# Performance work log

Measured on AMD Instinct MI355X. Metric: run time of the kernel, lower is better.

Reference implementation:

```python
import jax, jax.numpy as jnp
import numpy as np

B, D, H = 16384, 2048, 16
EPS = 1e-5


def setup_inputs() -> dict:
    key = jax.random.key(0)
    ks = jax.random.split(key, 14)
    s = 0.02
    return {
        "e_a": jax.random.normal(ks[0], (B, D), jnp.float32),
        "e_b": jax.random.normal(ks[1], (B, D), jnp.float32),
        "w_in_ab": jax.random.normal(ks[2], (3 * D, D), jnp.float32) * s,
        "b_in_ab": jnp.zeros((3 * D,), jnp.float32),
        "w_out_ab": jax.random.normal(ks[3], (D, D), jnp.float32) * s,
        "b_out_ab": jnp.zeros((D,), jnp.float32),
        "w_in_ba": jax.random.normal(ks[4], (3 * D, D), jnp.float32) * s,
        "b_in_ba": jnp.zeros((3 * D,), jnp.float32),
        "w_out_ba": jax.random.normal(ks[5], (D, D), jnp.float32) * s,
        "b_out_ba": jnp.zeros((D,), jnp.float32),
        "gamma_a": jnp.ones((D,), jnp.float32),
        "beta_a": jnp.zeros((D,), jnp.float32),
        "gamma_b": jnp.ones((D,), jnp.float32),
        "beta_b": jnp.zeros((D,), jnp.float32),
    }


def _mha_seq1(q_in, kv_in, w_in, b_in, w_out, b_out):
    """torch nn.MultiheadAttention with seq_len=1 for both query and key."""
    b, d = q_in.shape
    hd = d // H
    wq, wk, wv = jnp.split(w_in, 3, axis=0)
    bq, bk, bv = jnp.split(b_in, 3)
    q = (q_in @ wq.T + bq).reshape(b, H, hd)
    k = (kv_in @ wk.T + bk).reshape(b, H, hd)
    v = (kv_in @ wv.T + bv).reshape(b, H, hd)
    scores = jnp.sum(q * k, axis=-1) / jnp.sqrt(jnp.asarray(hd, q.dtype))  # (B,H)
    w = jax.nn.softmax(scores[..., None], axis=-1)  # (B,H,1) == ones (single key)
    attn = (w * v).reshape(b, d)
    out = attn @ w_out.T + b_out
    attn_w = jnp.mean(w, axis=1)[:, None, :]  # (B,1,1), averaged over heads
    return out, attn_w


def _layernorm(x, g, b):
    m = jnp.mean(x, axis=-1, keepdims=True)
    v = jnp.mean((x - m) ** 2, axis=-1, keepdims=True)
    return (x - m) / jnp.sqrt(v + EPS) * g + b


def reference(e_a, e_b, w_in_ab, b_in_ab, w_out_ab, b_out_ab,
              w_in_ba, b_in_ba, w_out_ba, b_out_ba,
              gamma_a, beta_a, gamma_b, beta_b):
    a_attn, attn_w_a = _mha_seq1(e_a, e_b, w_in_ab, b_in_ab, w_out_ab, b_out_ab)
    b_attn, _ = _mha_seq1(e_b, e_a, w_in_ba, b_in_ba, w_out_ba, b_out_ba)
    e_a_prime = _layernorm(e_a + a_attn, gamma_a, beta_a)
    e_b_prime = _layernorm(e_b + b_attn, gamma_b, beta_b)
    return (e_a_prime, e_b_prime, attn_w_a)
```

## Files before the change

### kernel.cpp

```cpp
#include <hip/hip_runtime.h>
#include <hip/hip_bf16.h>
#include <stdint.h>
#include <stddef.h>


static constexpr int B_ROWS = 16384;
static constexpr int DIM    = 2048;
static constexpr float EPS  = 1e-5f;

typedef __bf16 bf16_t;
typedef __bf16 bf16x8 __attribute__((ext_vector_type(8)));
typedef float  f32x4  __attribute__((ext_vector_type(4)));

__global__ __launch_bounds__(256) void k_f32_to_bf16(const float* __restrict__ in,
                                                     bf16_t* __restrict__ out) {
  size_t i = ((size_t)blockIdx.x * 256 + threadIdx.x) * 8;
  f32x4 a = *(const f32x4*)(in + i);
  f32x4 b = *(const f32x4*)(in + i + 4);
  bf16x8 o;
  o[0] = (bf16_t)a[0]; o[1] = (bf16_t)a[1]; o[2] = (bf16_t)a[2]; o[3] = (bf16_t)a[3];
  o[4] = (bf16_t)b[0]; o[5] = (bf16_t)b[1]; o[6] = (bf16_t)b[2]; o[7] = (bf16_t)b[3];
  *(bf16x8*)(out + i) = o;
}

__global__ __launch_bounds__(256) void k_transpose_bf16(const float* __restrict__ W,
                                                        bf16_t* __restrict__ Wt,
                                                        int n) {
  __shared__ float t[32][33];
  const int bx = blockIdx.x * 32, by = blockIdx.y * 32;
  const int tx = threadIdx.x & 31, ty = threadIdx.x >> 5;
  #pragma unroll
  for (int r = ty; r < 32; r += 8)
    t[r][tx] = W[(size_t)(by + r) * n + bx + tx];
  __syncthreads();
  #pragma unroll
  for (int r = ty; r < 32; r += 8)
    Wt[(size_t)(bx + r) * n + by + tx] = (bf16_t)t[tx][r];
}

__global__ __launch_bounds__(256) void k_bias_combine(const float* __restrict__ wout,
                                                      const float* __restrict__ bv,
                                                      const float* __restrict__ bout,
                                                      float* __restrict__ bc, int n) {
  const int i = blockIdx.x;
  const float* row = wout + (size_t)i * n;
  float s = 0.f;
  for (int k = threadIdx.x; k < n; k += 256) s += row[k] * bv[k];
  #pragma unroll
  for (int o = 32; o; o >>= 1) s += __shfl_down(s, o, 64);
  __shared__ float red[4];
  if ((threadIdx.x & 63) == 0) red[threadIdx.x >> 6] = s;
  __syncthreads();
  if (threadIdx.x == 0) bc[i] = red[0] + red[1] + red[2] + red[3] + bout[i];
}

__device__ inline void gld_lds16(const bf16_t* g, bf16_t* l) {
  __builtin_amdgcn_global_load_lds(
      (const __attribute__((address_space(1))) void*)g,
      (__attribute__((address_space(3))) void*)l, 16, 0, 0);
}

template <int MODE>
__global__ __launch_bounds__(256) void k_gemm_bt(const bf16_t* __restrict__ A,
                                                 const bf16_t* __restrict__ Bt,
                                                 float* __restrict__ Cf,
                                                 bf16_t* __restrict__ Cb,
                                                 const float* __restrict__ resid,
                                                 const float* __restrict__ bias,
                                                 int M, int N, int K) {
  __shared__ bf16_t lA[128 * 32];
  __shared__ bf16_t lB[128 * 32];
  const int tid  = threadIdx.x;
  const int lane = tid & 63;
  const int wid  = tid >> 6;
  const int wm = wid >> 1, wn = wid & 1;

  int bx, by;
  if (MODE == 1) {
    const int nbx = N >> 7;
    const int nwg = (M >> 7) * nbx;
    const int orig = blockIdx.y * nbx + blockIdx.x;
    const int cpx = nwg >> 3;
    const int swz = (orig & 7) * cpx + (orig >> 3);
    bx = swz % nbx;
    by = swz / nbx;
  } else {
    bx = blockIdx.x;
    by = blockIdx.y;
  }
  const int m0 = by * 128, n0 = bx * 128;

  const int sr = tid >> 2;
  const int sc = (tid & 3) * 8;
  const bf16_t* gA0 = A  + (size_t)(m0 + sr) * K + sc;
  const bf16_t* gA1 = A  + (size_t)(m0 + 64 + sr) * K + sc;
  const bf16_t* gB0 = Bt + (size_t)(n0 + sr) * K + sc;
  const bf16_t* gB1 = Bt + (size_t)(n0 + 64 + sr) * K + sc;

  f32x4 acc[4][4] = {};

  const int fr = lane & 15;
  const int kh = (lane >> 4) * 8;

  for (int kt = 0; kt < K; kt += 32) {
    gld_lds16(gA0 + kt, lA + tid * 8);
    gld_lds16(gA1 + kt, lA + 2048 + tid * 8);
    gld_lds16(gB0 + kt, lB + tid * 8);
    gld_lds16(gB1 + kt, lB + 2048 + tid * 8);
    __syncthreads();

    bf16x8 af[4], bfv[4];
    #pragma unroll
    for (int i = 0; i < 4; ++i) {
      af[i]  = *(const bf16x8*)(lA + (wm * 64 + i * 16 + fr) * 32 + kh);
      bfv[i] = *(const bf16x8*)(lB + (wn * 64 + i * 16 + fr) * 32 + kh);
    }
    #pragma unroll
    for (int i = 0; i < 4; ++i)
      #pragma unroll
      for (int j = 0; j < 4; ++j)
        acc[i][j] = __builtin_amdgcn_mfma_f32_16x16x32_bf16(af[i], bfv[j], acc[i][j], 0, 0, 0);
    __syncthreads();
  }

  const int cr = (lane >> 4) * 4;
  const int cc = lane & 15;
  #pragma unroll
  for (int i = 0; i < 4; ++i) {
    #pragma unroll
    for (int j = 0; j < 4; ++j) {
      const int gm = m0 + wm * 64 + i * 16 + cr;
      const int gn = n0 + wn * 64 + j * 16 + cc;
      #pragma unroll
      for (int r = 0; r < 4; ++r) {
        const size_t idx = (size_t)(gm + r) * N + gn;
        if (MODE == 0) {
          Cb[idx] = (bf16_t)acc[i][j][r];
        } else {
          Cf[idx] = acc[i][j][r] + resid[idx] + bias[gn];
        }
      }
    }
  }
}

__global__ __launch_bounds__(256) void k_ln(float* __restrict__ io,
                                            const float* __restrict__ gamma_a,
                                            const float* __restrict__ beta_a,
                                            const float* __restrict__ gamma_b,
                                            const float* __restrict__ beta_b) {
  const int row = blockIdx.x;
  const float* gamma = (row < B_ROWS) ? gamma_a : gamma_b;
  const float* beta  = (row < B_ROWS) ? beta_a  : beta_b;
  float* p = io + (size_t)row * DIM;
  const int c0 = threadIdx.x * 8;

  f32x4 x0 = *(f32x4*)(p + c0);
  f32x4 x1 = *(f32x4*)(p + c0 + 4);
  float s = 0.f, sq = 0.f;
  #pragma unroll
  for (int r = 0; r < 4; ++r) {
    s += x0[r] + x1[r];
    sq += x0[r] * x0[r] + x1[r] * x1[r];
  }
  #pragma unroll
  for (int o = 32; o; o >>= 1) {
    s  += __shfl_down(s, o, 64);
    sq += __shfl_down(sq, o, 64);
  }
  __shared__ float rs[4], rq[4];
  if ((threadIdx.x & 63) == 0) { rs[threadIdx.x >> 6] = s; rq[threadIdx.x >> 6] = sq; }
  __syncthreads();
  s  = rs[0] + rs[1] + rs[2] + rs[3];
  sq = rq[0] + rq[1] + rq[2] + rq[3];

  const float mean = s * (1.f / DIM);
  const float var  = sq * (1.f / DIM) - mean * mean;
  const float inv  = rsqrtf(var + EPS);

  f32x4 g0 = *(const f32x4*)(gamma + c0);
  f32x4 g1 = *(const f32x4*)(gamma + c0 + 4);
  f32x4 b0 = *(const f32x4*)(beta + c0);
  f32x4 b1 = *(const f32x4*)(beta + c0 + 4);
  #pragma unroll
  for (int r = 0; r < 4; ++r) {
    x0[r] = (x0[r] - mean) * inv * g0[r] + b0[r];
    x1[r] = (x1[r] - mean) * inv * g1[r] + b1[r];
  }
  *(f32x4*)(p + c0)     = x0;
  *(f32x4*)(p + c0 + 4) = x1;
}

__global__ __launch_bounds__(256) void k_fill_ones(float* __restrict__ p, int n) {
  const int i = blockIdx.x * 256 + threadIdx.x;
  if (i < n) p[i] = 1.0f;
}

extern "C" void kernel_launch(void* const* d_in, const int* in_sizes, int n_in,
                              void* d_out, int out_size, void* d_ws, size_t ws_size,
                              hipStream_t stream) {
  const float* e_a      = (const float*)d_in[0];
  const float* e_b      = (const float*)d_in[1];
  const float* w_in_ab  = (const float*)d_in[2];
  const float* b_in_ab  = (const float*)d_in[3];
  const float* w_out_ab = (const float*)d_in[4];
  const float* b_out_ab = (const float*)d_in[5];
  const float* w_in_ba  = (const float*)d_in[6];
  const float* b_in_ba  = (const float*)d_in[7];
  const float* w_out_ba = (const float*)d_in[8];
  const float* b_out_ba = (const float*)d_in[9];
  const float* gamma_a  = (const float*)d_in[10];
  const float* beta_a   = (const float*)d_in[11];
  const float* gamma_b  = (const float*)d_in[12];
  const float* beta_b   = (const float*)d_in[13];
  float* out = (float*)d_out;

  char* w = (char*)d_ws;
  bf16_t* eA_bf  = (bf16_t*)w; w += (size_t)B_ROWS * DIM * 2;
  bf16_t* eB_bf  = (bf16_t*)w; w += (size_t)B_ROWS * DIM * 2;
  bf16_t* woAB   = (bf16_t*)w; w += (size_t)DIM * DIM * 2;
  bf16_t* woBA   = (bf16_t*)w; w += (size_t)DIM * DIM * 2;
  bf16_t* wvTAB  = (bf16_t*)w; w += (size_t)DIM * DIM * 2;
  bf16_t* wvTBA  = (bf16_t*)w; w += (size_t)DIM * DIM * 2;
  bf16_t* wcAB   = (bf16_t*)w; w += (size_t)DIM * DIM * 2;
  bf16_t* wcBA   = (bf16_t*)w; w += (size_t)DIM * DIM * 2;
  float*  bcAB   = (float*)w;  w += (size_t)DIM * 4;
  float*  bcBA   = (float*)w;  w += (size_t)DIM * 4;

  const size_t nE = (size_t)B_ROWS * DIM;
  const size_t nW = (size_t)DIM * DIM;

  k_f32_to_bf16<<<nE / 2048, 256, 0, stream>>>(e_a, eA_bf);
  k_f32_to_bf16<<<nE / 2048, 256, 0, stream>>>(e_b, eB_bf);
  k_f32_to_bf16<<<nW / 2048, 256, 0, stream>>>(w_out_ab, woAB);
  k_f32_to_bf16<<<nW / 2048, 256, 0, stream>>>(w_out_ba, woBA);
  k_transpose_bf16<<<dim3(64, 64), 256, 0, stream>>>(w_in_ab + 2 * nW, wvTAB, DIM);
  k_transpose_bf16<<<dim3(64, 64), 256, 0, stream>>>(w_in_ba + 2 * nW, wvTBA, DIM);
  k_bias_combine<<<DIM, 256, 0, stream>>>(w_out_ab, b_in_ab + 2 * DIM, b_out_ab, bcAB, DIM);
  k_bias_combine<<<DIM, 256, 0, stream>>>(w_out_ba, b_in_ba + 2 * DIM, b_out_ba, bcBA, DIM);

  k_gemm_bt<0><<<dim3(16, 16), 256, 0, stream>>>(woAB, wvTAB, nullptr, wcAB,
                                                 nullptr, nullptr, DIM, DIM, DIM);
  k_gemm_bt<0><<<dim3(16, 16), 256, 0, stream>>>(woBA, wvTBA, nullptr, wcBA,
                                                 nullptr, nullptr, DIM, DIM, DIM);

  k_gemm_bt<1><<<dim3(16, 128), 256, 0, stream>>>(eB_bf, wcAB, out, nullptr,
                                                  e_a, bcAB, B_ROWS, DIM, DIM);
  k_gemm_bt<1><<<dim3(16, 128), 256, 0, stream>>>(eA_bf, wcBA, out + nE, nullptr,
                                                  e_b, bcBA, B_ROWS, DIM, DIM);

  k_ln<<<2 * B_ROWS, 256, 0, stream>>>(out, gamma_a, beta_a, gamma_b, beta_b);

  k_fill_ones<<<(B_ROWS + 255) / 256, 256, 0, stream>>>(out + 2 * nE, B_ROWS);
}
```

Measured before the change: 1.247 ms.

## Replace main GEMM with 256x256 double-buffered LDS-swizzled 8-wave kernel

Splits the GEMM into a small kernel for the weight-combine products and a new 256x256-tile, 512-thread kernel for the two large B x D products. The new kernel uses K=64 steps, double-buffered LDS filled by direct global-to-LDS loads, an XOR swizzle to avoid bank conflicts, and interleaves next-tile prefetch with MFMA phases using explicit barriers, vmcnt waits and setprio. The aim is to raise data reuse per tile and hide global-load latency behind matrix math. In exchange it uses 128 KB of LDS per block and hand-placed waits, so a misplaced vmcnt could cause a race or stall.

```diff
diff --git a/kernel.cpp b/kernel.cpp
--- a/kernel.cpp
+++ b/kernel.cpp
@@ -11,6 +11,17 @@
 typedef __bf16 bf16_t;
 typedef __bf16 bf16x8 __attribute__((ext_vector_type(8)));
 typedef float  f32x4  __attribute__((ext_vector_type(4)));
+
+#define MEMFENCE asm volatile("" ::: "memory")
+#define SBAR     __builtin_amdgcn_s_barrier()
+#define SCHEDB   __builtin_amdgcn_sched_barrier(0)
+#define WAITVM(n) asm volatile("s_waitcnt vmcnt(" #n ")" ::: "memory")
+
+__device__ __forceinline__ void gld_lds16(const bf16_t* g, bf16_t* l) {
+  __builtin_amdgcn_global_load_lds(
+      (const __attribute__((address_space(1))) void*)g,
+      (__attribute__((address_space(3))) void*)l, 16, 0, 0);
+}
 
 __global__ __launch_bounds__(256) void k_f32_to_bf16(const float* __restrict__ in,
                                                      bf16_t* __restrict__ out) {
@@ -54,41 +65,17 @@
   if (threadIdx.x == 0) bc[i] = red[0] + red[1] + red[2] + red[3] + bout[i];
 }
 
-__device__ inline void gld_lds16(const bf16_t* g, bf16_t* l) {
-  __builtin_amdgcn_global_load_lds(
-      (const __attribute__((address_space(1))) void*)g,
-      (__attribute__((address_space(3))) void*)l, 16, 0, 0);
-}
-
-template <int MODE>
-__global__ __launch_bounds__(256) void k_gemm_bt(const bf16_t* __restrict__ A,
-                                                 const bf16_t* __restrict__ Bt,
-                                                 float* __restrict__ Cf,
-                                                 bf16_t* __restrict__ Cb,
-                                                 const float* __restrict__ resid,
-                                                 const float* __restrict__ bias,
-                                                 int M, int N, int K) {
+__global__ __launch_bounds__(256) void k_gemm_bt_small(const bf16_t* __restrict__ A,
+                                                       const bf16_t* __restrict__ Bt,
+                                                       bf16_t* __restrict__ Cb,
+                                                       int M, int N, int K) {
   __shared__ bf16_t lA[128 * 32];
   __shared__ bf16_t lB[128 * 32];
   const int tid  = threadIdx.x;
   const int lane = tid & 63;
   const int wid  = tid >> 6;
   const int wm = wid >> 1, wn = wid & 1;
-
-  int bx, by;
-  if (MODE == 1) {
-    const int nbx = N >> 7;
-    const int nwg = (M >> 7) * nbx;
-    const int orig = blockIdx.y * nbx + blockIdx.x;
-    const int cpx = nwg >> 3;
-    const int swz = (orig & 7) * cpx + (orig >> 3);
-    bx = swz % nbx;
-    by = swz / nbx;
-  } else {
-    bx = blockIdx.x;
-    by = blockIdx.y;
-  }
-  const int m0 = by * 128, n0 = bx * 128;
+  const int m0 = blockIdx.y * 128, n0 = blockIdx.x * 128;
 
   const int sr = tid >> 2;
   const int sc = (tid & 3) * 8;
@@ -98,7 +85,6 @@
   const bf16_t* gB1 = Bt + (size_t)(n0 + 64 + sr) * K + sc;
 
   f32x4 acc[4][4] = {};
-
   const int fr = lane & 15;
   const int kh = (lane >> 4) * 8;
 
@@ -108,7 +94,6 @@
     gld_lds16(gB0 + kt, lB + tid * 8);
     gld_lds16(gB1 + kt, lB + 2048 + tid * 8);
     __syncthreads();
-
     bf16x8 af[4], bfv[4];
     #pragma unroll
     for (int i = 0; i < 4; ++i) {
@@ -122,26 +107,196 @@
         acc[i][j] = __builtin_amdgcn_mfma_f32_16x16x32_bf16(af[i], bfv[j], acc[i][j], 0, 0, 0);
     __syncthreads();
   }
-
   const int cr = (lane >> 4) * 4;
   const int cc = lane & 15;
   #pragma unroll
-  for (int i = 0; i < 4; ++i) {
+  for (int i = 0; i < 4; ++i)
     #pragma unroll
     for (int j = 0; j < 4; ++j) {
       const int gm = m0 + wm * 64 + i * 16 + cr;
       const int gn = n0 + wn * 64 + j * 16 + cc;
       #pragma unroll
+      for (int r = 0; r < 4; ++r)
+        Cb[(size_t)(gm + r) * N + gn] = (bf16_t)acc[i][j][r];
+    }
+}
+
+__global__ __launch_bounds__(512, 2) void k_gemm256(const bf16_t* __restrict__ A,
+                                                    const bf16_t* __restrict__ Bt,
+                                                    float* __restrict__ Cf,
+                                                    const float* __restrict__ resid,
+                                                    const float* __restrict__ bias,
+                                                    int M, int N, int K) {
+  __shared__ bf16_t lA[2][256 * 64];
+  __shared__ bf16_t lB[2][256 * 64];
+  const int tid  = threadIdx.x;
+  const int lane = tid & 63;
+  const int wid  = tid >> 6;
+  const int wr = wid >> 2;
+  const int wc = wid & 3;
+
+  const int nbx = N >> 8;
+  const int nwg = (M >> 8) * nbx;
+  const int orig = blockIdx.y * nbx + blockIdx.x;
+  const int cpx = nwg >> 3;
+  const int swz = (orig & 7) * cpx + (orig >> 3);
+  const int m0 = (swz / nbx) << 8;
+  const int n0 = (swz % nbx) << 8;
+
+  const int srow  = tid >> 3;
+  const int sunit = (tid & 7) ^ ((tid >> 3) & 7);
+  const bf16_t* gA = A  + (size_t)(m0 + srow) * K + sunit * 8;
+  const bf16_t* gB = Bt + (size_t)(n0 + srow) * K + sunit * 8;
+  const size_t cK = (size_t)64 * K;
+  const int lofs = tid * 8;
+
+  f32x4 acc[8][4] = {};
+
+  const int NT = K >> 6;
+
+  const int frl = lane & 15;
+  const int fxor = lane & 7;
+  const int fg  = lane >> 4;
+
+#define LDA(buf, i, kk) \
+  (*(const bf16x8*)(&lA[buf][(wr * 128 + (i) * 16 + frl) * 64 + \
+                            ((((kk) * 4 + fg) ^ fxor) * 8)]))
+#define LDB(buf, j, kk) \
+  (*(const bf16x8*)(&lB[buf][(wc * 64 + (j) * 16 + frl) * 64 + \
+                            ((((kk) * 4 + fg) ^ fxor) * 8)]))
+#define STAGE_A(buf, c, kt) gld_lds16(gA + (size_t)(c) * cK + (kt), \
+                                      &lA[buf][(c) * 4096 + lofs])
+#define STAGE_B(buf, c, kt) gld_lds16(gB + (size_t)(c) * cK + (kt), \
+                                      &lB[buf][(c) * 4096 + lofs])
+
+#define MFMA16(mg, kk)                                                         \
+  __builtin_amdgcn_s_setprio(1);                                               \
+  _Pragma("unroll")                                                            \
+  for (int mi = 0; mi < 4; ++mi) {                                             \
+    _Pragma("unroll")                                                          \
+    for (int j = 0; j < 4; ++j)                                                \
+      acc[(mg) * 4 + mi][j] = __builtin_amdgcn_mfma_f32_16x16x32_bf16(         \
+          af[mi], bf[j], acc[(mg) * 4 + mi][j], 0, 0, 0);                      \
+  }                                                                            \
+  __builtin_amdgcn_s_setprio(0)
+
+  {
+    STAGE_B(0, 0, 0); STAGE_B(0, 1, 0); STAGE_B(0, 2, 0); STAGE_B(0, 3, 0);
+    STAGE_A(0, 0, 0); STAGE_A(0, 2, 0); STAGE_A(0, 1, 0); STAGE_A(0, 3, 0);
+    WAITVM(0); SCHEDB;
+    MEMFENCE; SBAR; MEMFENCE;
+  }
+
+  bf16x8 bf[4];
+  int buf = 0;
+
+  for (int t = 0; t < NT - 1; ++t) {
+    const int ktn = (t + 1) << 6;
+    const int nb = buf ^ 1;
+    {
+      bf16x8 af[4];
+      #pragma unroll
+      for (int mi = 0; mi < 4; ++mi) af[mi] = LDA(buf, mi, 0);
+      #pragma unroll
+      for (int j = 0; j < 4; ++j) bf[j] = LDB(buf, j, 0);
+      STAGE_B(nb, 0, ktn); STAGE_B(nb, 1, ktn);
+      MEMFENCE; SBAR; MEMFENCE;
+      MFMA16(0, 0);
+      WAITVM(2); SCHEDB;
+      MEMFENCE; SBAR; MEMFENCE;
+    }
+    {
+      bf16x8 af[4];
+      #pragma unroll
+      for (int mi = 0; mi < 4; ++mi) af[mi] = LDA(buf, 4 + mi, 0);
+      STAGE_B(nb, 2, ktn); STAGE_B(nb, 3, ktn);
+      MEMFENCE; SBAR; MEMFENCE;
+      MFMA16(1, 0);
+      MEMFENCE; SBAR; MEMFENCE;
+    }
+    {
+      bf16x8 af[4];
+      #pragma unroll
+      for (int mi = 0; mi < 4; ++mi) af[mi] = LDA(buf, mi, 1);
+      #pragma unroll
+      for (int j = 0; j < 4; ++j) bf[j] = LDB(buf, j, 1);
+      STAGE_A(nb, 0, ktn); STAGE_A(nb, 2, ktn);
+      MEMFENCE; SBAR; MEMFENCE;
+      MFMA16(0, 1);
+      MEMFENCE; SBAR; MEMFENCE;
+    }
+    {
+      bf16x8 af[4];
+      #pragma unroll
+      for (int mi = 0; mi < 4; ++mi) af[mi] = LDA(buf, 4 + mi, 1);
+      STAGE_A(nb, 1, ktn); STAGE_A(nb, 3, ktn);
+      MEMFENCE; SBAR; MEMFENCE;
+      MFMA16(1, 1);
+      WAITVM(2); SCHEDB;
+      MEMFENCE; SBAR; MEMFENCE;
+    }
+    buf = nb;
+  }
+
+  {
+    {
+      bf16x8 af[4];
+      #pragma unroll
+      for (int mi = 0; mi < 4; ++mi) af[mi] = LDA(buf, mi, 0);
+      #pragma unroll
+      for (int j = 0; j < 4; ++j) bf[j] = LDB(buf, j, 0);
+      MEMFENCE; SBAR; MEMFENCE;
+      MFMA16(0, 0);
+      WAITVM(0); SCHEDB;
+      MEMFENCE; SBAR; MEMFENCE;
+    }
+    {
+      bf16x8 af[4];
+      #pragma unroll
+      for (int mi = 0; mi < 4; ++mi) af[mi] = LDA(buf, 4 + mi, 0);
+      MEMFENCE; SBAR; MEMFENCE;
+      MFMA16(1, 0);
+      MEMFENCE; SBAR; MEMFENCE;
+    }
+    {
+      bf16x8 af[4];
+      #pragma unroll
+      for (int mi = 0; mi < 4; ++mi) af[mi] = LDA(buf, mi, 1);
+      #pragma unroll
+      for (int j = 0; j < 4; ++j) bf[j] = LDB(buf, j, 1);
+      MEMFENCE; SBAR; MEMFENCE;
+      MFMA16(0, 1);
+      MEMFENCE; SBAR; MEMFENCE;
+    }
+    {
+      bf16x8 af[4];
+      #pragma unroll
+      for (int mi = 0; mi < 4; ++mi) af[mi] = LDA(buf, 4 + mi, 1);
+      MEMFENCE; SBAR; MEMFENCE;
+      MFMA16(1, 1);
+    }
+  }
+
+  const int cr = (lane >> 4) * 4;
+  const int cc = lane & 15;
+  #pragma unroll
+  for (int i = 0; i < 8; ++i) {
+    #pragma unroll
+    for (int j = 0; j < 4; ++j) {
+      const int gm = m0 + wr * 128 + i * 16 + cr;
+      const int gn = n0 + wc * 64 + j * 16 + cc;
+      #pragma unroll
       for (int r = 0; r < 4; ++r) {
         const size_t idx = (size_t)(gm + r) * N + gn;
-        if (MODE == 0) {
-          Cb[idx] = (bf16_t)acc[i][j][r];
-        } else {
-          Cf[idx] = acc[i][j][r] + resid[idx] + bias[gn];
-        }
+        Cf[idx] = acc[i][j][r] + resid[idx] + bias[gn];
       }
     }
   }
+#undef LDA
+#undef LDB
+#undef STAGE_A
+#undef STAGE_B
+#undef MFMA16
 }
 
 __global__ __launch_bounds__(256) void k_ln(float* __restrict__ io,
@@ -239,15 +394,13 @@
   k_bias_combine<<<DIM, 256, 0, stream>>>(w_out_ab, b_in_ab + 2 * DIM, b_out_ab, bcAB, DIM);
   k_bias_combine<<<DIM, 256, 0, stream>>>(w_out_ba, b_in_ba + 2 * DIM, b_out_ba, bcBA, DIM);
 
-  k_gemm_bt<0><<<dim3(16, 16), 256, 0, stream>>>(woAB, wvTAB, nullptr, wcAB,
-                                                 nullptr, nullptr, DIM, DIM, DIM);
-  k_gemm_bt<0><<<dim3(16, 16), 256, 0, stream>>>(woBA, wvTBA, nullptr, wcBA,
-                                                 nullptr, nullptr, DIM, DIM, DIM);
-
-  k_gemm_bt<1><<<dim3(16, 128), 256, 0, stream>>>(eB_bf, wcAB, out, nullptr,
-                                                  e_a, bcAB, B_ROWS, DIM, DIM);
-  k_gemm_bt<1><<<dim3(16, 128), 256, 0, stream>>>(eA_bf, wcBA, out + nE, nullptr,
-                                                  e_b, bcBA, B_ROWS, DIM, DIM);
+  k_gemm_bt_small<<<dim3(16, 16), 256, 0, stream>>>(woAB, wvTAB, wcAB, DIM, DIM, DIM);
+  k_gemm_bt_small<<<dim3(16, 16), 256, 0, stream>>>(woBA, wvTBA, wcBA, DIM, DIM, DIM);
+
+  k_gemm256<<<dim3(8, 64), 512, 0, stream>>>(eB_bf, wcAB, out,      e_a, bcAB,
+                                             B_ROWS, DIM, DIM);
+  k_gemm256<<<dim3(8, 64), 512, 0, stream>>>(eA_bf, wcBA, out + nE, e_b, bcBA,
+                                             B_ROWS, DIM, DIM);
 
   k_ln<<<2 * B_ROWS, 256, 0, stream>>>(out, gamma_a, beta_a, gamma_b, beta_b);
 
```

Measured after the change: 1.071 ms. 1.16x faster.
